# Kernel tuning notes

Measured on AMD Instinct MI355X. Metric: run time of the kernel, lower is better.

## Reference

```python
import jax, jax.numpy as jnp
import numpy as np

B, NT, D, V = 16, 4096, 512, 2545  # batch, text len, text_dim, text_num_embeds


def setup_inputs() -> dict:
    key = jax.random.key(0)
    k_txt, k_len, k_emb = jax.random.split(key, 3)
    text = jax.random.randint(k_txt, (B, NT), 0, V, dtype=jnp.int64)
    # ragged valid lengths; pad tail with -1 (-> token 0 after +1 shift)
    lengths = jax.random.randint(k_len, (B,), 1, NT + 1, dtype=jnp.int64)
    pos = jnp.arange(NT, dtype=jnp.int64)
    text = jnp.where(pos[None, :] < lengths[:, None], text, -1)
    emb = jax.random.normal(k_emb, (V + 1, D), dtype=jnp.float32) * 0.02
    return {"text": text, "seq_len": 4096, "emb": emb}


def _forward(emb, text, seq_len):
    t = text + 1
    t = t[:, :seq_len]
    t = jnp.pad(t, ((0, 0), (0, seq_len - t.shape[1])))  # pad with 0
    pad_mask = t == 0                      # [b, s] True at padding
    x = emb[t]                             # [b, s, d] embedding lookup
    # --- average upsample by valid mask (vectorized replacement of the
    #     per-batch Python loop in average_upsample_text_by_mask) ---
    valid = ~pad_mask
    L = valid.sum(axis=1)                  # [b] valid token counts
    # stable argsort of ~valid puts valid positions first, in order
    order = jnp.argsort(~valid, axis=1, stable=True)        # [b, s]
    gathered = jnp.take_along_axis(x, order[:, :, None], axis=1)  # [b, s, d]
    Ls = jnp.maximum(L, 1)
    base = seq_len // Ls                   # [b]
    rem = seq_len % Ls                     # [b]
    # token j repeats base times for j < L-rem, base+1 times for j >= L-rem
    pos = jnp.arange(seq_len, dtype=L.dtype)                # [s]
    boundary = (Ls - rem) * base           # [b] first output pos of the +1 block
    j_lo = pos[None, :] // base[:, None]
    j_hi = (Ls - rem)[:, None] + (pos[None, :] - boundary[:, None]) // (base + 1)[:, None]
    j = jnp.where(pos[None, :] < boundary[:, None], j_lo, j_hi)  # [b, s]
    out = jnp.take_along_axis(gathered, j[:, :, None], axis=1)   # [b, s, d]
    out = jnp.where((L == 0)[:, None, None], jnp.zeros((), out.dtype), out)
    return out


def reference(text, seq_len, emb):
    return _forward(emb, text, seq_len)
```

## Files before the change

### kernel.cpp

```cpp
#include <hip/hip_runtime.h>

#define B_   16
#define NT_  4096
#define D_   512
#define CHUNK 256

typedef float f4 __attribute__((ext_vector_type(4)));

__global__ __launch_bounds__(256) void compact_kernel(const int* __restrict__ text,
                                                      int* __restrict__ tok,
                                                      int* __restrict__ meta) {
    const int b = blockIdx.x >> 4;
    const int c = blockIdx.x & 15;
    const int t = threadIdx.x;
    const int lane = t & 63;
    const int wid  = t >> 6;
    const int* row = text + b * NT_;

    int pre = 0;
    for (int i = t; i < c * CHUNK; i += 256) pre += (row[i] >= 0) ? 1 : 0;
    #pragma unroll
    for (int off = 32; off > 0; off >>= 1) pre += __shfl_down(pre, off, 64);
    __shared__ int s_pre[4];
    if (lane == 0) s_pre[wid] = pre;
    __syncthreads();
    const int chunk_base = s_pre[0] + s_pre[1] + s_pre[2] + s_pre[3];

    const int v = row[c * CHUNK + t];
    const int pred = (v >= 0) ? 1 : 0;
    int x = pred;
    #pragma unroll
    for (int off = 1; off < 64; off <<= 1) {
        int y = __shfl_up(x, off, 64);
        if (lane >= off) x += y;
    }
    __shared__ int s_wsum[4];
    if (lane == 63) s_wsum[wid] = x;
    __syncthreads();
    int woff = 0;
    for (int w = 0; w < wid; ++w) woff += s_wsum[w];

    if (pred) tok[b * NT_ + chunk_base + woff + (x - pred)] = v + 1;

    if (c == 15 && t == 255) {
        const int L  = chunk_base + woff + x;
        const int Ls = (L > 0) ? L : 1;
        const int base = NT_ / Ls;
        const int rem  = NT_ % Ls;
        meta[b * 4 + 0] = L;
        meta[b * 4 + 1] = base;
        meta[b * 4 + 2] = rem;
        meta[b * 4 + 3] = (Ls - rem) * base;
    }
}

__global__ __launch_bounds__(256) void expand_fused(const f4* __restrict__ emb,
                                                    const int* __restrict__ tok,
                                                    const int* __restrict__ meta,
                                                    f4* __restrict__ out) {
    const int t     = threadIdx.x;
    const int pidx0 = blockIdx.x << 4;
    const int b     = pidx0 >> 12;

    __shared__ int s_tok[16];
    if (t < 16) {
        const int p = (pidx0 & (NT_ - 1)) + t;
        const int L = meta[b * 4 + 0];
        int tkn = -1;
        if (L > 0) {
            const int base     = meta[b * 4 + 1];
            const int rem      = meta[b * 4 + 2];
            const int boundary = meta[b * 4 + 3];
            const int j = (p < boundary) ? (p / base)
                                         : ((L - rem) + (p - boundary) / (base + 1));
            tkn = tok[b * NT_ + j];
        }
        s_tok[t] = tkn;
    }
    __syncthreads();

    const size_t obase = (size_t)pidx0 * (D_ / 4);
    #pragma unroll
    for (int k = 0; k < 8; ++k) {
        const int f   = k * 256 + t;
        const int pl  = f >> 7;
        const int d4  = f & 127;
        const int tkn = s_tok[pl];
        f4 v;
        if (tkn < 0) {
            v = (f4){0.f, 0.f, 0.f, 0.f};
        } else {
            v = emb[(size_t)tkn * (D_ / 4) + d4];
        }
        __builtin_nontemporal_store(v, &out[obase + f]);
    }
}

extern "C" void kernel_launch(void* const* d_in, const int* in_sizes, int n_in,
                              void* d_out, int out_size, void* d_ws, size_t ws_size,
                              hipStream_t stream) {
    const int*   text = (const int*)d_in[0];
    const float* emb  = (const float*)d_in[2];
    f4*          out  = (f4*)d_out;

    int* tok  = (int*)d_ws;
    int* meta = tok + B_ * NT_;

    compact_kernel<<<B_ * 16, 256, 0, stream>>>(text, tok, meta);
    expand_fused<<<(B_ * NT_) / 16, 256, 0, stream>>>(
        (const f4*)emb, tok, meta, out);
}
```

Baseline: 158.8 us.

## Fuse compaction and expansion into one kernel via per-block row prefix scan

Replaces the separate compaction kernel and the workspace token and metadata buffers with a single kernel. Each block recounts valid tokens over its whole batch row, builds a prefix table in shared memory, and binary-searches it to find each source token. This removes a kernel launch and the global dependency between the two kernels. In exchange, every block redundantly reads and scans the full 4096-entry text row, which adds L2 traffic and latency before the output stores.

```diff
diff --git a/kernel.cpp b/kernel.cpp
--- a/kernel.cpp
+++ b/kernel.cpp
@@ -3,32 +3,24 @@
 #define B_   16
 #define NT_  4096
 #define D_   512
-#define CHUNK 256
 
 typedef float f4 __attribute__((ext_vector_type(4)));
 
-__global__ __launch_bounds__(256) void compact_kernel(const int* __restrict__ text,
-                                                      int* __restrict__ tok,
-                                                      int* __restrict__ meta) {
-    const int b = blockIdx.x >> 4;
-    const int c = blockIdx.x & 15;
-    const int t = threadIdx.x;
-    const int lane = t & 63;
-    const int wid  = t >> 6;
-    const int* row = text + b * NT_;
+__global__ __launch_bounds__(256) void fused_all(const int* __restrict__ text,
+                                                 const f4* __restrict__ emb,
+                                                 f4* __restrict__ out) {
+    const int t     = threadIdx.x;
+    const int lane  = t & 63;
+    const int wid   = t >> 6;
+    const int pidx0 = blockIdx.x << 4;
+    const int b     = pidx0 >> 12;
+    const int* row  = text + b * NT_;
 
-    int pre = 0;
-    for (int i = t; i < c * CHUNK; i += 256) pre += (row[i] >= 0) ? 1 : 0;
+    int cnt = 0;
     #pragma unroll
-    for (int off = 32; off > 0; off >>= 1) pre += __shfl_down(pre, off, 64);
-    __shared__ int s_pre[4];
-    if (lane == 0) s_pre[wid] = pre;
-    __syncthreads();
-    const int chunk_base = s_pre[0] + s_pre[1] + s_pre[2] + s_pre[3];
+    for (int k = 0; k < 16; ++k) cnt += (row[t * 16 + k] >= 0) ? 1 : 0;
 
-    const int v = row[c * CHUNK + t];
-    const int pred = (v >= 0) ? 1 : 0;
-    int x = pred;
+    int x = cnt;
     #pragma unroll
     for (int off = 1; off < 64; off <<= 1) {
         int y = __shfl_up(x, off, 64);
@@ -39,41 +31,37 @@
     __syncthreads();
     int woff = 0;
     for (int w = 0; w < wid; ++w) woff += s_wsum[w];
+    const int L = s_wsum[0] + s_wsum[1] + s_wsum[2] + s_wsum[3];
 
-    if (pred) tok[b * NT_ + chunk_base + woff + (x - pred)] = v + 1;
-
-    if (c == 15 && t == 255) {
-        const int L  = chunk_base + woff + x;
-        const int Ls = (L > 0) ? L : 1;
-        const int base = NT_ / Ls;
-        const int rem  = NT_ % Ls;
-        meta[b * 4 + 0] = L;
-        meta[b * 4 + 1] = base;
-        meta[b * 4 + 2] = rem;
-        meta[b * 4 + 3] = (Ls - rem) * base;
-    }
-}
-
-__global__ __launch_bounds__(256) void expand_fused(const f4* __restrict__ emb,
-                                                    const int* __restrict__ tok,
-                                                    const int* __restrict__ meta,
-                                                    f4* __restrict__ out) {
-    const int t     = threadIdx.x;
-    const int pidx0 = blockIdx.x << 4;
-    const int b     = pidx0 >> 12;
+    __shared__ int s_pref[256];
+    s_pref[t] = woff + x;
+    __syncthreads();
 
     __shared__ int s_tok[16];
     if (t < 16) {
-        const int p = (pidx0 & (NT_ - 1)) + t;
-        const int L = meta[b * 4 + 0];
         int tkn = -1;
         if (L > 0) {
-            const int base     = meta[b * 4 + 1];
-            const int rem      = meta[b * 4 + 2];
-            const int boundary = meta[b * 4 + 3];
+            const int base     = NT_ / L;
+            const int rem      = NT_ % L;
+            const int boundary = (L - rem) * base;
+            const int p = (pidx0 & (NT_ - 1)) + t;
             const int j = (p < boundary) ? (p / base)
                                          : ((L - rem) + (p - boundary) / (base + 1));
-            tkn = tok[b * NT_ + j];
+            int lo = 0, hi = 255;
+            while (lo < hi) {
+                const int mid = (lo + hi) >> 1;
+                if (s_pref[mid] > j) hi = mid; else lo = mid + 1;
+            }
+            const int s = lo;
+            int r = j - ((s > 0) ? s_pref[s - 1] : 0);
+            const int* strip = row + s * 16;
+            for (int k = 0; k < 16; ++k) {
+                const int v = strip[k];
+                if (v >= 0) {
+                    if (r == 0) { tkn = v + 1; break; }
+                    --r;
+                }
+            }
         }
         s_tok[t] = tkn;
     }
@@ -82,15 +70,13 @@
     const size_t obase = (size_t)pidx0 * (D_ / 4);
     #pragma unroll
     for (int k = 0; k < 8; ++k) {
-        const int f   = k * 256 + t;
-        const int pl  = f >> 7;
-        const int d4  = f & 127;
-        const int tkn = s_tok[pl];
+        const int f   = (k << 8) + t;
+        const int tkn = s_tok[f >> 7];
         f4 v;
         if (tkn < 0) {
             v = (f4){0.f, 0.f, 0.f, 0.f};
         } else {
-            v = emb[(size_t)tkn * (D_ / 4) + d4];
+            v = emb[(size_t)tkn * (D_ / 4) + (f & 127)];
         }
         __builtin_nontemporal_store(v, &out[obase + f]);
     }
@@ -103,10 +89,6 @@
     const float* emb  = (const float*)d_in[2];
     f4*          out  = (f4*)d_out;
 
-    int* tok  = (int*)d_ws;
-    int* meta = tok + B_ * NT_;
-
-    compact_kernel<<<B_ * 16, 256, 0, stream>>>(text, tok, meta);
-    expand_fused<<<(B_ * NT_) / 16, 256, 0, stream>>>(
-        (const f4*)emb, tok, meta, out);
+    fused_all<<<(B_ * NT_) / 16, 256, 0, stream>>>(
+        text, (const f4*)emb, out);
 }
```

Result: no change. 156.0 us (-1.8%).
